# Performance work log

Measured on AMD Instinct MI355X. Metric: run time of the kernel, lower is better.

The kernel has to match this reference:

```python
import jax, jax.numpy as jnp
import numpy as np

B, P = 8, 768
S = 36                 # sample_points (also deformable offset pairs)
C_IN, C_ADJ = 64, 72   # prior_feat_channels -> adjusted channels
D, G = 512, 4          # fc_hidden_dim, num_groups (= attention heads)
N_OFFSETS, N_STRIPS, DEG = 72, 71, 3


def _bilinear(img, x, y):
    """img: [B,H,W,C]; x,y: [B,N] pixel coords. Bilinear sample, zeros outside."""
    H, W = img.shape[1], img.shape[2]
    x0 = jnp.floor(x); y0 = jnp.floor(y)
    x0i = x0.astype(jnp.int32); y0i = y0.astype(jnp.int32)
    wx1 = x - x0; wy1 = y - y0

    def corner(xi, yi, w):
        valid = (xi >= 0) & (xi < W) & (yi >= 0) & (yi < H)
        xc = jnp.clip(xi, 0, W - 1); yc = jnp.clip(yi, 0, H - 1)
        vals = jax.vmap(lambda f, yy, xx: f[yy, xx])(img, yc, xc)  # [B,N,C]
        return vals * (w * valid)[..., None]

    return (corner(x0i, y0i, (1 - wx1) * (1 - wy1))
            + corner(x0i + 1, y0i, wx1 * (1 - wy1))
            + corner(x0i, y0i + 1, (1 - wx1) * wy1)
            + corner(x0i + 1, y0i + 1, wx1 * wy1))


def _resize_ac(img, Ht, Wt):
    """Bilinear resize with align_corners=True. img: [B,H,W,C]."""
    Bsz, H, W, _ = img.shape
    gy, gx = jnp.meshgrid(jnp.linspace(0.0, H - 1.0, Ht),
                          jnp.linspace(0.0, W - 1.0, Wt), indexing='ij')
    xf = jnp.broadcast_to(gx.reshape(-1), (Bsz, Ht * Wt))
    yf = jnp.broadcast_to(gy.reshape(-1), (Bsz, Ht * Wt))
    return _bilinear(img, xf, yf).reshape(Bsz, Ht, Wt, -1)


def setup_inputs():
    ks = jax.random.split(jax.random.key(0), 32)
    r = lambda i, shp, s=1.0: jax.random.normal(ks[i], shp, dtype=jnp.float32) * s
    z = lambda shp: jnp.zeros(shp, jnp.float32)
    return {
        'feat0': r(0, (B, C_IN, 40, 100)),
        'feat1': r(1, (B, C_IN, 20, 50)),
        'feat2': r(2, (B, C_IN, 10, 25)),
        'priors': jax.random.uniform(ks[3], (B, P, 4 + N_OFFSETS), dtype=jnp.float32) * N_STRIPS,
        'ca_w': r(4, (C_ADJ, C_IN), 0.125), 'ca_b': z((C_ADJ,)),
        'off_w': r(5, (2 * S, C_ADJ), 0.01), 'off_b': r(6, (2 * S,), 0.01),
        'dp_w': r(7, (C_ADJ, C_ADJ), 0.167), 'dp_b': z((C_ADJ,)),
        'z_emb': r(8, (S,), 0.3) + 1.0,
        'gf_w': r(9, (D, S // G, C_ADJ), 0.02), 'gf_b': z((D,)),
        'wq': r(10, (D, D), 0.044), 'bq': z((D,)),
        'wk': r(11, (D, D), 0.044), 'bk': z((D,)),
        'wv': r(12, (D, D), 0.044), 'bv': z((D,)),
        'wo': r(13, (D, D), 0.044), 'bo': z((D,)),
        'cf_w1': r(14, (2 * D, D), 0.044), 'cf_b1': z((2 * D,)),
        'cf_w2': r(15, (D, 2 * D), 0.031), 'cf_b2': z((D,)),
        'cls_w1': r(16, (D, D), 0.044), 'cls_b1': z((D,)),
        'cls_w2': r(17, (2, D), 0.001), 'cls_b2': z((2,)),
        'reg_w1': r(18, (D, D), 0.044), 'reg_b1': z((D,)),
        'p_w1': r(19, (2 * D, D), 0.044), 'p_b1': z((2 * D,)),
        'p_w2': r(20, (DEG + 1, 2 * D), 0.031), 'p_b2': z((DEG + 1,)),
        'b_scale': jnp.ones((1,), jnp.float32), 'b_bias': z((1,)),
    }


def reference(feat0, feat1, feat2, priors, ca_w, ca_b, off_w, off_b, dp_w, dp_b,
              z_emb, gf_w, gf_b, wq, bq, wk, bk, wv, bv, wo, bo,
              cf_w1, cf_b1, cf_w2, cf_b2, cls_w1, cls_b1, cls_w2, cls_b2,
              reg_w1, reg_b1, p_w1, p_b1, p_w2, p_b2, b_scale, b_bias):
    f32 = jnp.float32
    lin = lambda x, w, b: x @ w.T + b

    # ---- prior sampling grid (CLRNet-style) ----
    sx_idx = jnp.floor(jnp.linspace(0.0, 1.0, S) * N_STRIPS).astype(jnp.int32)
    pf_ys = jnp.flip(1.0 - sx_idx.astype(f32) / N_STRIPS)            # [S]
    pf_xs = priors[..., 4 + sx_idx][:, :, ::-1]                       # [B,P,S]
    gx = jnp.clip(pf_xs / N_STRIPS, 0.0, 1.0) * 2.0 - 1.0            # [-1,1]
    gy = jnp.broadcast_to(pf_ys * 2.0 - 1.0, gx.shape)

    # ---- channel adjust (1x1 conv) per level, channels-last ----
    adj = lambda f: jnp.einsum('bchw,oc->bhwo', f, ca_w) + ca_b
    feats = [adj(feat0), adj(feat1), adj(feat2)]                      # [B,H,W,C_ADJ]
    offs0 = jnp.einsum('bhwc,oc->bhwo', feats[0], off_w) + off_b     # [B,H0,W0,2S]

    # ---- deformable multi-level sampling: per (prior, point) gather + 1x1 proj ----
    sidx = jnp.arange(S)
    levels = []
    for l, fl in enumerate(feats):
        Hl, Wl = fl.shape[1], fl.shape[2]
        offs = offs0 if l == 0 else _resize_ac(offs0, Hl, Wl)
        px = (gx + 1.0) * 0.5 * (Wl - 1)
        py = (gy + 1.0) * 0.5 * (Hl - 1)
        ov = _bilinear(offs, px.reshape(B, -1), py.reshape(B, -1)).reshape(B, P, S, S, 2)
        dyx = ov[:, :, sidx, sidx, :]                                 # offset pair s for point s
        sxp = (px + dyx[..., 1]).reshape(B, -1)
        syp = (py + dyx[..., 0]).reshape(B, -1)
        smp = _bilinear(fl, sxp, syp).reshape(B, P, S, C_ADJ)
        levels.append(smp @ dp_w.T + dp_b)
    feat_all = jnp.stack(levels)                                      # [3,B,P,S,C]

    # ---- z-embedding soft level selection ----
    zw = jax.nn.softmax(-(z_emb[:, None] - jnp.arange(3, dtype=f32)) ** 2 / 2.0, axis=-1)  # [S,3]
    feature = jnp.einsum('lbpsc,sl->bpsc', feat_all, zw)

    # ---- grouped gather Conv1d(S -> D, kernel=C_ADJ, groups=G) ----
    xg = feature.reshape(B * P, G, S // G, C_ADJ)
    wg = gf_w.reshape(G, D // G, S // G, C_ADJ)
    feature = (jnp.einsum('ngik,goik->ngo', xg, wg).reshape(B * P, D) + gf_b).reshape(B, P, D)

    # ---- multi-head self-attention over priors + channel MLP residual ----
    dh = D // G
    q = lin(feature, wq, bq).reshape(B, P, G, dh).transpose(0, 2, 1, 3)
    k = lin(feature, wk, bk).reshape(B, P, G, dh).transpose(0, 2, 1, 3)
    v = lin(feature, wv, bv).reshape(B, P, G, dh).transpose(0, 2, 1, 3)
    attn = jax.nn.softmax(jnp.einsum('bgqd,bgkd->bgqk', q, k) / float(np.sqrt(dh)), axis=-1)
    res = jnp.einsum('bgqk,bgkd->bgqd', attn, v).transpose(0, 2, 1, 3).reshape(B, P, D)
    res = lin(res, wo, bo)
    feature = feature + lin(jax.nn.relu(lin(res, cf_w1, cf_b1)), cf_w2, cf_b2)

    # ---- heads ----
    fc = feature.reshape(B * P, D)
    cls_logits = lin(jax.nn.relu(lin(fc, cls_w1, cls_b1)), cls_w2, cls_b2).reshape(B, P, 2)
    reg = jax.nn.relu(lin(fc, reg_w1, reg_b1)).reshape(B, P, D)
    coeffs = lin(jax.nn.relu(lin(reg, p_w1, p_b1)), p_w2, p_b2)       # [B,P,DEG+1]
    coeffs = jnp.concatenate([coeffs[..., :2], coeffs[..., 2:] * b_scale + b_bias], axis=-1)
    ys = jnp.linspace(0.0, 1.0, N_OFFSETS)
    basis = jnp.stack([ys ** i for i in range(DEG + 1)], axis=1)      # [N_OFFSETS, DEG+1]
    xs_pred = jax.nn.sigmoid(jnp.einsum('bnd,od->bno', coeffs, basis))
    return jnp.concatenate([cls_logits, coeffs, xs_pred], axis=-1)    # [B,P,78]
```

## Files before the change

### kernel.cpp

```cpp
#include <hip/hip_runtime.h>
#include <hip/hip_bf16.h>
#include <math.h>

#define BB 8
#define PP 768
#define NPRI 76
#define SS 36
#define CIN 64
#define CADJ 72
#define DD 512

#define H0 40
#define W0 100
#define H1 20
#define W1 50
#define H2 10
#define W2 25

typedef __attribute__((ext_vector_type(8))) short bf16x8;
typedef __attribute__((ext_vector_type(4))) short bf16x4;
typedef __attribute__((ext_vector_type(4))) float f32x4;
#define MFMA_BF16 __builtin_amdgcn_mfma_f32_16x16x32_bf16

typedef const __attribute__((address_space(1))) unsigned int* gas_t;
typedef __attribute__((address_space(3))) unsigned int* las_t;

__device__ __forceinline__ __hip_bfloat16 to_bf16(float v) { return __float2bfloat16(v); }
__device__ __forceinline__ float bf2f(__hip_bfloat16 v) { return __bfloat162float(v); }
__device__ __forceinline__ short to_bf16s(float v) {
    __hip_bfloat16 h = __float2bfloat16(v);
    return *reinterpret_cast<short*>(&h);
}
__device__ __forceinline__ float bfs2f(short s) {
    union { unsigned u; float f; } cv;
    cv.u = ((unsigned)(unsigned short)s) << 16;
    return cv.f;
}

__device__ __forceinline__ float bsample(const float* __restrict__ img, int H, int W,
                                         int C, int c, float x, float y)
{
    float x0f = floorf(x), y0f = floorf(y);
    int x0 = (int)x0f, y0 = (int)y0f;
    float wx1 = x - x0f, wy1 = y - y0f;
    float wx0 = 1.0f - wx1, wy0 = 1.0f - wy1;
    int xc0 = min(max(x0, 0), W - 1);
    int xc1 = min(max(x0 + 1, 0), W - 1);
    int yc0 = min(max(y0, 0), H - 1);
    int yc1 = min(max(y0 + 1, 0), H - 1);
    bool vx0 = (x0 >= 0) && (x0 < W);
    bool vx1 = (x0 + 1 >= 0) && (x0 + 1 < W);
    bool vy0 = (y0 >= 0) && (y0 < H);
    bool vy1 = (y0 + 1 >= 0) && (y0 + 1 < H);
    float w00 = (vx0 && vy0) ? wx0 * wy0 : 0.0f;
    float w01 = (vx1 && vy0) ? wx1 * wy0 : 0.0f;
    float w10 = (vx0 && vy1) ? wx0 * wy1 : 0.0f;
    float w11 = (vx1 && vy1) ? wx1 * wy1 : 0.0f;
    return w00 * img[((size_t)yc0 * W + xc0) * C + c]
         + w01 * img[((size_t)yc0 * W + xc1) * C + c]
         + w10 * img[((size_t)yc1 * W + xc0) * C + c]
         + w11 * img[((size_t)yc1 * W + xc1) * C + c];
}

__global__ __launch_bounds__(256) void k_wprep(
    const float* __restrict__ wq, const float* __restrict__ wk, const float* __restrict__ wv,
    const float* __restrict__ wo, const float* __restrict__ cf_w1, const float* __restrict__ cf_w2,
    const float* __restrict__ cls_w1, const float* __restrict__ reg_w1, const float* __restrict__ p_w1,
    const float* __restrict__ bq, const float* __restrict__ bk, const float* __restrict__ bv,
    const float* __restrict__ cls_b1, const float* __restrict__ reg_b1,
    const float* __restrict__ gf_w, const float* __restrict__ dp_w,
    const float* __restrict__ dp_b, const float* __restrict__ gf_b,
    __hip_bfloat16* __restrict__ wqkv, __hip_bfloat16* __restrict__ wo_bf,
    __hip_bfloat16* __restrict__ cf1_bf, __hip_bfloat16* __restrict__ cf2_bf,
    __hip_bfloat16* __restrict__ clsreg_bf, __hip_bfloat16* __restrict__ p1_bf,
    __hip_bfloat16* __restrict__ gfw2, float* __restrict__ b2,
    float* __restrict__ bqkv, float* __restrict__ bclsreg)
{
    __shared__ float dpS[CADJ][CADJ + 1];
    __shared__ float gfr[648];
    const int bid = blockIdx.x;
    const int tid = threadIdx.x;

    if (bid < 512) {
        const int o = bid;
        for (int i = tid; i < CADJ * CADJ; i += 256) dpS[i / CADJ][i % CADJ] = dp_w[i];
        for (int i = tid; i < 648; i += 256) gfr[i] = gf_w[(size_t)o * 648 + i];
        __syncthreads();
        for (int t = tid; t < 672; t += 256) {
            float acc = 0.0f;
            if (t < 648) {
                const int i = t / 72, m = t % 72;
                const float* gr = gfr + i * 72;
#pragma unroll 8
                for (int k = 0; k < 72; ++k) acc = fmaf(gr[k], dpS[k][m], acc);
            }
            gfw2[(size_t)o * 672 + t] = to_bf16(acc);
        }
        return;
    }
    if (bid < 514) {
        const int o = (bid - 512) * 256 + tid;
        if (o < DD) {
            const float* gr = gf_w + (size_t)o * 648;
            float acc = gf_b[o];
            for (int j = 0; j < 648; ++j) acc = fmaf(gr[j], dp_b[j % 72], acc);
            b2[o] = acc;
        }
        return;
    }
    long i = (long)(bid - 514) * 256 + tid;
    if (i < 262144) { wqkv[i] = to_bf16(wq[i]); return; }
    i -= 262144;
    if (i < 262144) { wqkv[262144 + i] = to_bf16(wk[i]); return; }
    i -= 262144;
    if (i < 262144) { wqkv[524288 + i] = to_bf16(wv[i]); return; }
    i -= 262144;
    if (i < 262144) { wo_bf[i] = to_bf16(wo[i]); return; }
    i -= 262144;
    if (i < 524288) { cf1_bf[i] = to_bf16(cf_w1[i]); return; }
    i -= 524288;
    if (i < 524288) { cf2_bf[i] = to_bf16(cf_w2[i]); return; }
    i -= 524288;
    if (i < 262144) { clsreg_bf[i] = to_bf16(cls_w1[i]); return; }
    i -= 262144;
    if (i < 262144) { clsreg_bf[262144 + i] = to_bf16(reg_w1[i]); return; }
    i -= 262144;
    if (i < 524288) { p1_bf[i] = to_bf16(p_w1[i]); return; }
    i -= 524288;
    if (i < 512) { bqkv[i] = bq[i]; return; }
    if (i < 1024) { bqkv[i] = bk[i - 512]; return; }
    if (i < 1536) { bqkv[i] = bv[i - 1024]; return; }
    i -= 1536;
    if (i < 512) { bclsreg[i] = cls_b1[i]; return; }
    if (i < 1024) { bclsreg[i] = reg_b1[i - 512]; return; }
}

__global__ __launch_bounds__(256) void k_adjoff(
    const float* __restrict__ f, const float* __restrict__ caw, const float* __restrict__ cab,
    const float* __restrict__ offw, const float* __restrict__ offb,
    __hip_bfloat16* __restrict__ feout, float* __restrict__ offout, int HW, int do_off)
{
    __shared__ float inS[64][65];
    __shared__ float wS[72][64];
    __shared__ float owS[72][73];
    __shared__ float feS[64][73];
    __shared__ float cabS[72], obS[72];

    const int tid = threadIdx.x;
    const int b = blockIdx.y;
    const int pix0 = blockIdx.x * 64;
    const int cnt = min(64, HW - pix0);
    const int px = tid & 63, og = tid >> 6, o0 = og * 18;

    const float* fb = f + (size_t)b * CIN * HW + pix0;
    for (int i = tid; i < 72 * 64; i += 256) wS[i >> 6][i & 63] = caw[i];
    if (do_off)
        for (int i = tid; i < 72 * 72; i += 256) owS[i / 72][i % 72] = offw[i];
    if (tid < 72) { cabS[tid] = cab[tid]; obS[tid] = do_off ? offb[tid] : 0.f; }
    for (int i = tid; i < 64 * 64; i += 256) {
        const int c = i >> 6, p = i & 63;
        inS[c][p] = (p < cnt) ? fb[(size_t)c * HW + p] : 0.f;
    }
    __syncthreads();

    float acc[18];
#pragma unroll
    for (int j = 0; j < 18; ++j) acc[j] = cabS[o0 + j];
#pragma unroll 4
    for (int c = 0; c < 64; ++c) {
        const float v = inS[c][px];
#pragma unroll
        for (int j = 0; j < 18; ++j) acc[j] = fmaf(v, wS[o0 + j][c], acc[j]);
    }
#pragma unroll
    for (int j = 0; j < 18; ++j) feS[px][o0 + j] = acc[j];
    __syncthreads();

    __hip_bfloat16* feg = feout + ((size_t)b * HW + pix0) * CADJ;
    for (int i = tid; i < cnt * CADJ; i += 256) feg[i] = to_bf16(feS[i / CADJ][i % CADJ]);

    if (!do_off) return;

    float acc2[18];
#pragma unroll
    for (int j = 0; j < 18; ++j) acc2[j] = obS[o0 + j];
#pragma unroll 4
    for (int c = 0; c < 72; ++c) {
        const float v = feS[px][c];
#pragma unroll
        for (int j = 0; j < 18; ++j) acc2[j] = fmaf(v, owS[o0 + j][c], acc2[j]);
    }
    __syncthreads();
#pragma unroll
    for (int j = 0; j < 18; ++j) feS[px][o0 + j] = acc2[j];
    __syncthreads();
    float* ofg = offout + ((size_t)b * HW + pix0) * CADJ;
    for (int i = tid; i < cnt * CADJ; i += 256) ofg[i] = feS[i / CADJ][i % CADJ];
}

__global__ __launch_bounds__(256) void k_resize2(const float* __restrict__ src,
    float* __restrict__ of1, float* __restrict__ of2)
{
    const int T1 = BB * H1 * W1 * CADJ;
    const int T2 = BB * H2 * W2 * CADJ;
    int idx = blockIdx.x * 256 + threadIdx.x;
    if (idx < T1) {
        const int c = idx % CADJ;
        const int j = (idx / CADJ) % W1;
        const int i = (idx / (CADJ * W1)) % H1;
        const int b = idx / (CADJ * W1 * H1);
        float sy = fminf((float)i * ((float)(H0 - 1) / (float)(H1 - 1)), (float)(H0 - 1));
        float sx = fminf((float)j * ((float)(W0 - 1) / (float)(W1 - 1)), (float)(W0 - 1));
        of1[idx] = bsample(src + (size_t)b * H0 * W0 * CADJ, H0, W0, CADJ, c, sx, sy);
        return;
    }
    idx -= T1;
    if (idx >= T2) return;
    const int c = idx % CADJ;
    const int j = (idx / CADJ) % W2;
    const int i = (idx / (CADJ * W2)) % H2;
    const int b = idx / (CADJ * W2 * H2);
    float sy = fminf((float)i * ((float)(H0 - 1) / (float)(H2 - 1)), (float)(H0 - 1));
    float sx = fminf((float)j * ((float)(W0 - 1) / (float)(W2 - 1)), (float)(W0 - 1));
    of2[idx] = bsample(src + (size_t)b * H0 * W0 * CADJ, H0, W0, CADJ, c, sx, sy);
}

__global__ __launch_bounds__(256) void k_sample(
    const float* __restrict__ priors,
    const __hip_bfloat16* __restrict__ feats0, const __hip_bfloat16* __restrict__ feats1,
    const __hip_bfloat16* __restrict__ feats2,
    const float* __restrict__ offs0,  const float* __restrict__ offs1,  const float* __restrict__ offs2,
    const float* __restrict__ z_emb,
    __hip_bfloat16* __restrict__ fsout)
{
    const int bid = blockIdx.x;
    const int gi = (bid & 7) * 384 + (bid >> 3);
    const int bp0 = gi * 2;
    const int b = bp0 / PP;
    const int tid = threadIdx.x;

    __shared__ int   ib[2][3][SS][4];
    __shared__ float wz[2][3][SS][4];

    const int Hs[3] = {H0, H1, H2};
    const int Wsz[3] = {W0, W1, W2};
    const __hip_bfloat16* Fb[3] = { feats0 + (size_t)b * H0 * W0 * CADJ,
                                    feats1 + (size_t)b * H1 * W1 * CADJ,
                                    feats2 + (size_t)b * H2 * W2 * CADJ };
    const float* Ob[3] = { offs0 + (size_t)b * H0 * W0 * CADJ,
                           offs1 + (size_t)b * H1 * W1 * CADJ,
                           offs2 + (size_t)b * H2 * W2 * CADJ };

    if (tid < 2 * 3 * SS) {
        const int p = tid / 108;
        const int l = (tid % 108) / SS;
        const int s = tid % SS;
        const int bp = bp0 + p;
        const float t = (float)(35 - s) / 35.0f;
        const int m = (int)floorf(t * 71.0f);
        const float pfx = priors[(size_t)bp * NPRI + 4 + m];
        const float gxv = fminf(fmaxf(pfx / 71.0f, 0.0f), 1.0f) * 2.0f - 1.0f;
        const float gyv = (1.0f - (float)m / 71.0f) * 2.0f - 1.0f;
        const float z = z_emb[s];
        const float e0 = expf(-0.5f * z * z);
        const float e1 = expf(-0.5f * (z - 1.0f) * (z - 1.0f));
        const float e2 = expf(-0.5f * (z - 2.0f) * (z - 2.0f));
        const float inv = 1.0f / (e0 + e1 + e2);
        const float ev[3] = {e0, e1, e2};
        const float zwl = ev[l] * inv;

        const int Hl = Hs[l], Wl = Wsz[l];
        const float px = (gxv + 1.0f) * 0.5f * (float)(Wl - 1);
        const float py = (gyv + 1.0f) * 0.5f * (float)(Hl - 1);
        const float dy = bsample(Ob[l], Hl, Wl, CADJ, 2 * s,     px, py);
        const float dx = bsample(Ob[l], Hl, Wl, CADJ, 2 * s + 1, px, py);
        const float sx = px + dx, sy = py + dy;
        const float x0f = floorf(sx), y0f = floorf(sy);
        const int x0 = (int)x0f, y0 = (int)y0f;
        const float wx1 = sx - x0f, wy1 = sy - y0f;
        const float wx0 = 1.0f - wx1, wy0 = 1.0f - wy1;
        const bool vx0 = (x0 >= 0) && (x0 < Wl);
        const bool vx1 = (x0 + 1 >= 0) && (x0 + 1 < Wl);
        const bool vy0 = (y0 >= 0) && (y0 < Hl);
        const bool vy1 = (y0 + 1 >= 0) && (y0 + 1 < Hl);
        const int xc0 = min(max(x0, 0), Wl - 1);
        const int xc1 = min(max(x0 + 1, 0), Wl - 1);
        const int yc0 = min(max(y0, 0), Hl - 1);
        const int yc1 = min(max(y0 + 1, 0), Hl - 1);
        wz[p][l][s][0] = ((vx0 && vy0) ? wx0 * wy0 : 0.0f) * zwl;
        wz[p][l][s][1] = ((vx1 && vy0) ? wx1 * wy0 : 0.0f) * zwl;
        wz[p][l][s][2] = ((vx0 && vy1) ? wx0 * wy1 : 0.0f) * zwl;
        wz[p][l][s][3] = ((vx1 && vy1) ? wx1 * wy1 : 0.0f) * zwl;
        ib[p][l][s][0] = (yc0 * Wl + xc0) * CADJ;
        ib[p][l][s][1] = (yc0 * Wl + xc1) * CADJ;
        ib[p][l][s][2] = (yc1 * Wl + xc0) * CADJ;
        ib[p][l][s][3] = (yc1 * Wl + xc1) * CADJ;
    }
    __syncthreads();

    for (int idx = tid; idx < 2 * SS * 18; idx += 256) {
        const int p = idx / 648;
        const int rem = idx % 648;
        const int s = rem / 18, k4 = (rem % 18) * 4;
        float a0 = 0.f, a1 = 0.f, a2 = 0.f, a3 = 0.f;
#pragma unroll
        for (int l = 0; l < 3; ++l) {
            const __hip_bfloat16* F = Fb[l];
            const int*   ibs = ib[p][l][s];
            const float* ws  = wz[p][l][s];
#pragma unroll
            for (int c = 0; c < 4; ++c) {
                const bf16x4 v = *(const bf16x4*)(F + ibs[c] + k4);
                const float w = ws[c];
                a0 = fmaf(w, bfs2f(v[0]), a0);
                a1 = fmaf(w, bfs2f(v[1]), a1);
                a2 = fmaf(w, bfs2f(v[2]), a2);
                a3 = fmaf(w, bfs2f(v[3]), a3);
            }
        }
        bf16x4 pk;
        pk[0] = to_bf16s(a0); pk[1] = to_bf16s(a1);
        pk[2] = to_bf16s(a2); pk[3] = to_bf16s(a3);
        __hip_bfloat16* orow = fsout + (size_t)(bp0 + p) * 2688;
        *(bf16x4*)&orow[(s / 9) * 672 + (s % 9) * 72 + k4] = pk;
    }
    if (tid < 2 * 96) {
        const int p = tid / 96, g = (tid % 96) / 24, t = tid % 24;
        fsout[(size_t)(bp0 + p) * 2688 + g * 672 + 648 + t] = to_bf16(0.0f);
    }
}

__global__ __launch_bounds__(256) void k_bgemm(
    const __hip_bfloat16* __restrict__ A, int lda, long sAz,
    const __hip_bfloat16* __restrict__ W, int ldw, long sWz,
    const float* __restrict__ bias, int sBz,
    const __hip_bfloat16* __restrict__ Res, int ldres,
    __hip_bfloat16* __restrict__ C, int ldc, int sCz,
    int K, int relu)
{
    __shared__ __hip_bfloat16 As[128][32];
    __shared__ __hip_bfloat16 Bs[128][32];
    const int tid = threadIdx.x;
    const int lane = tid & 63, w = tid >> 6;
    const int wr = w >> 1, wc = w & 1;
    const int row16 = lane & 15, kg = lane >> 4;
    const int z = blockIdx.z;
    const int m0 = blockIdx.y * 128, n0 = blockIdx.x * 128;
    const __hip_bfloat16* Ab = A + (size_t)z * sAz;
    const __hip_bfloat16* Wb = W + (size_t)z * sWz;
    const int gr = lane >> 2;
    const int gc = (lane & 3) * 8;

    f32x4 acc[4][4];
#pragma unroll
    for (int i = 0; i < 4; ++i)
#pragma unroll
        for (int j = 0; j < 4; ++j) acc[i][j] = (f32x4){0.f, 0.f, 0.f, 0.f};

    for (int k0 = 0; k0 < K; k0 += 32) {
        __syncthreads();
#pragma unroll
        for (int c = 0; c < 2; ++c) {
            const int r = w * 32 + c * 16;
            __builtin_amdgcn_global_load_lds(
                (gas_t)(Ab + (size_t)(m0 + r + gr) * lda + k0 + gc),
                (las_t)&As[r][0], 16, 0, 0);
            __builtin_amdgcn_global_load_lds(
                (gas_t)(Wb + (size_t)(n0 + r + gr) * ldw + k0 + gc),
                (las_t)&Bs[r][0], 16, 0, 0);
        }
        __syncthreads();
        bf16x8 af[4], bfr[4];
#pragma unroll
        for (int i = 0; i < 4; ++i) af[i]  = *(const bf16x8*)&As[wr * 64 + i * 16 + row16][kg * 8];
#pragma unroll
        for (int j = 0; j < 4; ++j) bfr[j] = *(const bf16x8*)&Bs[wc * 64 + j * 16 + row16][kg * 8];
#pragma unroll
        for (int i = 0; i < 4; ++i)
#pragma unroll
            for (int j = 0; j < 4; ++j)
                acc[i][j] = MFMA_BF16(af[i], bfr[j], acc[i][j], 0, 0, 0);
    }

    const float* bz = bias + (size_t)z * sBz;
    __hip_bfloat16* Cz = C + (size_t)z * sCz;
#pragma unroll
    for (int i = 0; i < 4; ++i) {
#pragma unroll
        for (int r = 0; r < 4; ++r) {
            const int row = m0 + wr * 64 + i * 16 + kg * 4 + r;
#pragma unroll
            for (int j = 0; j < 4; ++j) {
                const int col = n0 + wc * 64 + j * 16 + row16;
                float v = acc[i][j][r] + bz[col];
                if (Res) v += bf2f(Res[(size_t)row * ldres + col]);
                if (relu) v = fmaxf(v, 0.0f);
                Cz[(size_t)row * ldc + col] = to_bf16(v);
            }
        }
    }
}

__global__ __launch_bounds__(256) void k_bgemm64(
    const __hip_bfloat16* __restrict__ A, int lda, long sAz,
    const __hip_bfloat16* __restrict__ W, int ldw, long sWz,
    const float* __restrict__ bias, int sBz,
    const __hip_bfloat16* __restrict__ Res, int ldres,
    __hip_bfloat16* __restrict__ C, int ldc, int sCz,
    int K, int relu)
{
    __shared__ __hip_bfloat16 As[2][64][32];
    __shared__ __hip_bfloat16 Bs[2][64][32];
    const int tid = threadIdx.x;
    const int lane = tid & 63, w = tid >> 6;
    const int wr = w >> 1, wc = w & 1;
    const int row16 = lane & 15, kg = lane >> 4;
    const int z = blockIdx.z;
    const int m0 = blockIdx.y * 64, n0 = blockIdx.x * 64;
    const __hip_bfloat16* Ab = A + (size_t)z * sAz;
    const __hip_bfloat16* Wb = W + (size_t)z * sWz;
    const int gr = lane >> 2;
    const int gc = (lane & 3) * 8;

    f32x4 acc[2][2];
#pragma unroll
    for (int i = 0; i < 2; ++i)
#pragma unroll
        for (int j = 0; j < 2; ++j) acc[i][j] = (f32x4){0.f, 0.f, 0.f, 0.f};

    __builtin_amdgcn_global_load_lds(
        (gas_t)(Ab + (size_t)(m0 + w * 16 + gr) * lda + gc),
        (las_t)&As[0][w * 16][0], 16, 0, 0);
    __builtin_amdgcn_global_load_lds(
        (gas_t)(Wb + (size_t)(n0 + w * 16 + gr) * ldw + gc),
        (las_t)&Bs[0][w * 16][0], 16, 0, 0);
    __syncthreads();

    int cur = 0;
    for (int k0 = 0; k0 < K; k0 += 32) {
        if (k0 + 32 < K) {
            const int nxt = cur ^ 1;
            __builtin_amdgcn_global_load_lds(
                (gas_t)(Ab + (size_t)(m0 + w * 16 + gr) * lda + k0 + 32 + gc),
                (las_t)&As[nxt][w * 16][0], 16, 0, 0);
            __builtin_amdgcn_global_load_lds(
                (gas_t)(Wb + (size_t)(n0 + w * 16 + gr) * ldw + k0 + 32 + gc),
                (las_t)&Bs[nxt][w * 16][0], 16, 0, 0);
        }
        bf16x8 af[2], bfr[2];
#pragma unroll
        for (int i = 0; i < 2; ++i) af[i]  = *(const bf16x8*)&As[cur][wr * 32 + i * 16 + row16][kg * 8];
#pragma unroll
        for (int j = 0; j < 2; ++j) bfr[j] = *(const bf16x8*)&Bs[cur][wc * 32 + j * 16 + row16][kg * 8];
#pragma unroll
        for (int i = 0; i < 2; ++i)
#pragma unroll
            for (int j = 0; j < 2; ++j)
                acc[i][j] = MFMA_BF16(af[i], bfr[j], acc[i][j], 0, 0, 0);
        __syncthreads();
        cur ^= 1;
    }

    const float* bz = bias + (size_t)z * sBz;
    __hip_bfloat16* Cz = C + (size_t)z * sCz;
#pragma unroll
    for (int i = 0; i < 2; ++i) {
#pragma unroll
        for (int r = 0; r < 4; ++r) {
            const int row = m0 + wr * 32 + i * 16 + kg * 4 + r;
#pragma unroll
            for (int j = 0; j < 2; ++j) {
                const int col = n0 + wc * 32 + j * 16 + row16;
                float v = acc[i][j][r] + bz[col];
                if (Res) v += bf2f(Res[(size_t)row * ldres + col]);
                if (relu) v = fmaxf(v, 0.0f);
                Cz[(size_t)row * ldc + col] = to_bf16(v);
            }
        }
    }
}

__global__ __launch_bounds__(256) void k_vt(
    const __hip_bfloat16* __restrict__ qkv, __hip_bfloat16* __restrict__ Vt)
{
    const int kt = blockIdx.x;
    const int bg = blockIdx.y;
    const int b = bg >> 2, g = bg & 3;
    const int tid = threadIdx.x;
    __shared__ unsigned short Vs[64][130];

    const __hip_bfloat16* src = qkv + (size_t)(b * PP + kt * 64) * 1536 + 1024 + g * 128;
    for (int i = tid; i < 1024; i += 256) {
        const int row = i >> 4, ch = i & 15;
        *(bf16x8*)&Vs[row][ch * 8] = *(const bf16x8*)(src + (size_t)row * 1536 + ch * 8);
    }
    __syncthreads();
    __hip_bfloat16* dst = Vt + (size_t)bg * 128 * 768 + kt * 64;
    for (int i = tid; i < 1024; i += 256) {
        const int d = i >> 3, kc = i & 7;
        bf16x8 pk;
#pragma unroll
        for (int j = 0; j < 8; ++j) pk[j] = (short)Vs[kc * 8 + j][d];
        *(bf16x8*)(dst + (size_t)d * 768 + kc * 8) = pk;
    }
}

__global__ __launch_bounds__(256) void k_fattn(
    const __hip_bfloat16* __restrict__ qkv, const __hip_bfloat16* __restrict__ Vt,
    __hip_bfloat16* __restrict__ Out)
{
    const int id = blockIdx.x;
    const int xcd = id & 7, rest = id >> 3;
    const int bg = xcd * 4 + rest / 12;
    const int qt = rest % 12;
    const int b = bg >> 2, g = bg & 3;
    const int tid = threadIdx.x, lane = tid & 63, w = tid >> 6;
    const int row16 = lane & 15, kg = lane >> 4;
    const int q0 = qt * 64;

    __shared__ __hip_bfloat16 Klds[64][136];
    __shared__ __hip_bfloat16 Vtl[128][72];
    __shared__ __hip_bfloat16 Plds[4][16][72];

    const size_t rowQ = (size_t)(b * PP + q0 + w * 16 + row16) * 1536 + g * 128;
    bf16x8 aq[4];
#pragma unroll
    for (int t = 0; t < 4; ++t)
        aq[t] = *(const bf16x8*)(qkv + rowQ + t * 32 + kg * 8);

    f32x4 oacc[8];
#pragma unroll
    for (int dt = 0; dt < 8; ++dt) oacc[dt] = (f32x4){0.f, 0.f, 0.f, 0.f};
    float mrow[4] = {-3.0e38f, -3.0e38f, -3.0e38f, -3.0e38f};
    float lrow[4] = {0.f, 0.f, 0.f, 0.f};

    const __hip_bfloat16* Kb = qkv + (size_t)(b * PP) * 1536 + 512 + g * 128;
    const __hip_bfloat16* Vb = Vt + (size_t)bg * 128 * 768;
    const float sc = 0.08838834764831845f;

    const int krow = tid >> 2, kch = tid & 3;
    const int vrow = tid >> 1, vch = tid & 1;
    bf16x8 kreg[4], vreg[4];

    {
        const __hip_bfloat16* s1 = Kb + (size_t)krow * 1536 + kch * 32;
        const __hip_bfloat16* s2 = Vb + (size_t)vrow * 768 + vch * 32;
#pragma unroll
        for (int j = 0; j < 4; ++j) { kreg[j] = *(const bf16x8*)(s1 + j * 8);
                                      vreg[j] = *(const bf16x8*)(s2 + j * 8); }
    }

    for (int kt = 0; kt < 12; ++kt) {
        __syncthreads();
#pragma unroll
        for (int j = 0; j < 4; ++j) {
            *(bf16x8*)&Klds[krow][kch * 32 + j * 8] = kreg[j];
            *(bf16x8*)&Vtl[vrow][vch * 32 + j * 8] = vreg[j];
        }
        __syncthreads();
        if (kt < 11) {
            const __hip_bfloat16* s1 = Kb + (size_t)((kt + 1) * 64 + krow) * 1536 + kch * 32;
            const __hip_bfloat16* s2 = Vb + (size_t)vrow * 768 + (kt + 1) * 64 + vch * 32;
#pragma unroll
            for (int j = 0; j < 4; ++j) { kreg[j] = *(const bf16x8*)(s1 + j * 8);
                                          vreg[j] = *(const bf16x8*)(s2 + j * 8); }
        }

        f32x4 s4[4];
#pragma unroll
        for (int st = 0; st < 4; ++st) s4[st] = (f32x4){0.f, 0.f, 0.f, 0.f};
        __builtin_amdgcn_s_setprio(1);
#pragma unroll
        for (int st = 0; st < 4; ++st)
#pragma unroll
            for (int t = 0; t < 4; ++t)
                s4[st] = MFMA_BF16(aq[t],
                    *(const bf16x8*)&Klds[st * 16 + row16][t * 32 + kg * 8], s4[st], 0, 0, 0);
        __builtin_amdgcn_s_setprio(0);

        float pm[4];
#pragma unroll
        for (int r = 0; r < 4; ++r) {
            float m0 = fmaxf(fmaxf(s4[0][r], s4[1][r]), fmaxf(s4[2][r], s4[3][r])) * sc;
            m0 = fmaxf(m0, __shfl_xor(m0, 1));
            m0 = fmaxf(m0, __shfl_xor(m0, 2));
            m0 = fmaxf(m0, __shfl_xor(m0, 4));
            m0 = fmaxf(m0, __shfl_xor(m0, 8));
            pm[r] = m0;
        }
        const float need = fmaxf(fmaxf(pm[0] - mrow[0], pm[1] - mrow[1]),
                                 fmaxf(pm[2] - mrow[2], pm[3] - mrow[3]));
        if (!__all(need <= 8.0f)) {
#pragma unroll
            for (int r = 0; r < 4; ++r) {
                const float mn = fmaxf(mrow[r], pm[r]);
                const float so = __expf(mrow[r] - mn);
                lrow[r] *= so;
#pragma unroll
                for (int dt = 0; dt < 8; ++dt) oacc[dt][r] *= so;
                mrow[r] = mn;
            }
        }
#pragma unroll
        for (int r = 0; r < 4; ++r) {
            float rs = 0.f;
#pragma unroll
            for (int st = 0; st < 4; ++st) {
                const float p = __expf(s4[st][r] * sc - mrow[r]);
                rs += p;
                Plds[w][kg * 4 + r][st * 16 + row16] = to_bf16(p);
            }
            rs += __shfl_xor(rs, 1);
            rs += __shfl_xor(rs, 2);
            rs += __shfl_xor(rs, 4);
            rs += __shfl_xor(rs, 8);
            lrow[r] += rs;
        }

        __builtin_amdgcn_s_setprio(1);
#pragma unroll
        for (int ks = 0; ks < 2; ++ks) {
            bf16x8 ap = *(const bf16x8*)&Plds[w][row16][ks * 32 + kg * 8];
#pragma unroll
            for (int dt = 0; dt < 8; ++dt)
                oacc[dt] = MFMA_BF16(ap,
                    *(const bf16x8*)&Vtl[dt * 16 + row16][ks * 32 + kg * 8], oacc[dt], 0, 0, 0);
        }
        __builtin_amdgcn_s_setprio(0);
    }

    const size_t obase = (size_t)(b * PP + q0 + w * 16 + kg * 4) * DD + g * 128;
#pragma unroll
    for (int r = 0; r < 4; ++r) {
        const float inv = 1.0f / lrow[r];
#pragma unroll
        for (int dt = 0; dt < 8; ++dt)
            Out[obase + (size_t)r * DD + dt * 16 + row16] = to_bf16(oacc[dt][r] * inv);
    }
}

__global__ __launch_bounds__(64) void k_head(
    const __hip_bfloat16* __restrict__ clsreg, const __hip_bfloat16* __restrict__ ph,
    const float* __restrict__ cls_w2, const float* __restrict__ cls_b2,
    const float* __restrict__ p_w2, const float* __restrict__ p_b2,
    const float* __restrict__ b_scale, const float* __restrict__ b_bias,
    float* __restrict__ outp)
{
    const int bp = blockIdx.x;
    const int lane = threadIdx.x;
    const __hip_bfloat16* hr = clsreg + (size_t)bp * 1024;
    float a0 = 0.0f, a1 = 0.0f;
    for (int i = lane; i < DD; i += 64) {
        float h = bf2f(hr[i]);
        a0 = fmaf(h, cls_w2[i], a0);
        a1 = fmaf(h, cls_w2[DD + i], a1);
    }
    const __hip_bfloat16* pr = ph + (size_t)bp * 1024;
    float c0 = 0.0f, c1 = 0.0f, c2 = 0.0f, c3 = 0.0f;
    for (int i = lane; i < 1024; i += 64) {
        float h = bf2f(pr[i]);
        c0 = fmaf(h, p_w2[i], c0);
        c1 = fmaf(h, p_w2[1024 + i], c1);
        c2 = fmaf(h, p_w2[2048 + i], c2);
        c3 = fmaf(h, p_w2[3072 + i], c3);
    }
#pragma unroll
    for (int off = 32; off > 0; off >>= 1) {
        a0 += __shfl_down(a0, off);
        a1 += __shfl_down(a1, off);
        c0 += __shfl_down(c0, off);
        c1 += __shfl_down(c1, off);
        c2 += __shfl_down(c2, off);
        c3 += __shfl_down(c3, off);
    }
    a0 = __shfl(a0, 0); a1 = __shfl(a1, 0);
    c0 = __shfl(c0, 0); c1 = __shfl(c1, 0);
    c2 = __shfl(c2, 0); c3 = __shfl(c3, 0);
    const float k0 = c0 + p_b2[0];
    const float k1 = c1 + p_b2[1];
    const float scv = b_scale[0], biv = b_bias[0];
    const float k2 = (c2 + p_b2[2]) * scv + biv;
    const float k3 = (c3 + p_b2[3]) * scv + biv;
    float* orow = outp + (size_t)bp * 78;
    if (lane == 0) {
        orow[0] = a0 + cls_b2[0];
        orow[1] = a1 + cls_b2[1];
        orow[2] = k0; orow[3] = k1; orow[4] = k2; orow[5] = k3;
    }
    for (int o = lane; o < 72; o += 64) {
        float ys = (float)o / 71.0f;
        float tv = k0 + ys * (k1 + ys * (k2 + ys * k3));
        orow[6 + o] = 1.0f / (1.0f + expf(-tv));
    }
}

extern "C" void kernel_launch(void* const* d_in, const int* in_sizes, int n_in,
                              void* d_out, int out_size, void* d_ws, size_t ws_size,
                              hipStream_t stream)
{
    const float* feat0  = (const float*)d_in[0];
    const float* feat1  = (const float*)d_in[1];
    const float* feat2  = (const float*)d_in[2];
    const float* priors = (const float*)d_in[3];
    const float* ca_w   = (const float*)d_in[4];
    const float* ca_b   = (const float*)d_in[5];
    const float* off_w  = (const float*)d_in[6];
    const float* off_b  = (const float*)d_in[7];
    const float* dp_w   = (const float*)d_in[8];
    const float* dp_b   = (const float*)d_in[9];
    const float* z_emb  = (const float*)d_in[10];
    const float* gf_w   = (const float*)d_in[11];
    const float* gf_b   = (const float*)d_in[12];
    const float* wq     = (const float*)d_in[13];
    const float* bq     = (const float*)d_in[14];
    const float* wk     = (const float*)d_in[15];
    const float* bk     = (const float*)d_in[16];
    const float* wv     = (const float*)d_in[17];
    const float* bv     = (const float*)d_in[18];
    const float* wo     = (const float*)d_in[19];
    const float* bo     = (const float*)d_in[20];
    const float* cf_w1  = (const float*)d_in[21];
    const float* cf_b1  = (const float*)d_in[22];
    const float* cf_w2  = (const float*)d_in[23];
    const float* cf_b2  = (const float*)d_in[24];
    const float* cls_w1 = (const float*)d_in[25];
    const float* cls_b1 = (const float*)d_in[26];
    const float* cls_w2 = (const float*)d_in[27];
    const float* cls_b2 = (const float*)d_in[28];
    const float* reg_w1 = (const float*)d_in[29];
    const float* reg_b1 = (const float*)d_in[30];
    const float* p_w1   = (const float*)d_in[31];
    const float* p_b1   = (const float*)d_in[32];
    const float* p_w2   = (const float*)d_in[33];
    const float* p_b2   = (const float*)d_in[34];
    const float* b_scale = (const float*)d_in[35];
    const float* b_bias  = (const float*)d_in[36];
    float* out = (float*)d_out;

    char* wsb = (char*)d_ws;
    __hip_bfloat16* feature = (__hip_bfloat16*)(wsb + 0);
    __hip_bfloat16* qkvb    = (__hip_bfloat16*)(wsb + 6291456);
    __hip_bfloat16* tb      = (__hip_bfloat16*)(wsb + 25165824);
    __hip_bfloat16* vtb     = (__hip_bfloat16*)(wsb + 31457280);
    __hip_bfloat16* rb      = (__hip_bfloat16*)(wsb + 31457280);
    __hip_bfloat16* hb      = (__hip_bfloat16*)(wsb + 37748736);
    __hip_bfloat16* f2      = (__hip_bfloat16*)(wsb + 50331648);
    __hip_bfloat16* clsregb = (__hip_bfloat16*)(wsb + 56623104);
    __hip_bfloat16* phb     = (__hip_bfloat16*)(wsb + 69206016);
    float* of1 = (float*)(wsb + 6291456);
    float* of2 = (float*)(wsb + 8595456);
    __hip_bfloat16* fe1 = (__hip_bfloat16*)(wsb + 9171456);
    __hip_bfloat16* fe2 = (__hip_bfloat16*)(wsb + 11475456);
    __hip_bfloat16* fsb = (__hip_bfloat16*)(wsb + 25165824);
    __hip_bfloat16* fe0 = (__hip_bfloat16*)(wsb + 58195968);
    float* of0 = (float*)(wsb + 67411968);
    __hip_bfloat16* wqkv_bf   = (__hip_bfloat16*)(wsb + 81788928);
    __hip_bfloat16* wo_bf     = (__hip_bfloat16*)(wsb + 83361792);
    __hip_bfloat16* cf1_bf    = (__hip_bfloat16*)(wsb + 83886080);
    __hip_bfloat16* cf2_bf    = (__hip_bfloat16*)(wsb + 84934656);
    __hip_bfloat16* clsreg_bf = (__hip_bfloat16*)(wsb + 85983232);
    __hip_bfloat16* p1_bf     = (__hip_bfloat16*)(wsb + 87031808);
    __hip_bfloat16* gfw2_bf   = (__hip_bfloat16*)(wsb + 88080384);
    float* bqkv    = (float*)(wsb + 88768512);
    float* bclsreg = (float*)(wsb + 88774656);
    float* b2      = (float*)(wsb + 88778752);

    k_wprep<<<12812, 256, 0, stream>>>(
        wq, wk, wv, wo, cf_w1, cf_w2, cls_w1, reg_w1, p_w1, bq, bk, bv, cls_b1, reg_b1,
        gf_w, dp_w, dp_b, gf_b,
        wqkv_bf, wo_bf, cf1_bf, cf2_bf, clsreg_bf, p1_bf, gfw2_bf, b2, bqkv, bclsreg);

    k_adjoff<<<dim3(63, BB), 256, 0, stream>>>(feat0, ca_w, ca_b, off_w, off_b,
                                               fe0, of0, H0 * W0, 1);
    k_adjoff<<<dim3(16, BB), 256, 0, stream>>>(feat1, ca_w, ca_b, off_w, off_b,
                                               fe1, nullptr, H1 * W1, 0);
    k_adjoff<<<dim3(4, BB), 256, 0, stream>>>(feat2, ca_w, ca_b, off_w, off_b,
                                              fe2, nullptr, H2 * W2, 0);
    k_resize2<<<(BB * (H1 * W1 + H2 * W2) * CADJ + 255) / 256, 256, 0, stream>>>(of0, of1, of2);
    k_sample<<<3072, 256, 0, stream>>>(priors, fe0, fe1, fe2, of0, of1, of2, z_emb, fsb);

    const int M = BB * PP;
    k_bgemm64<<<dim3(2, M / 64, 4), 256, 0, stream>>>(
        fsb, 2688, 672, gfw2_bf, 672, 128 * 672, b2, 128,
        nullptr, 0, feature, DD, 128, 672, 0);
    k_bgemm<<<dim3(12, M / 128, 1), 256, 0, stream>>>(
        feature, DD, 0, wqkv_bf, DD, 0, bqkv, 0,
        nullptr, 0, qkvb, 1536, 0, DD, 0);
    k_vt<<<dim3(12, 32), 256, 0, stream>>>(qkvb, vtb);
    k_fattn<<<384, 256, 0, stream>>>(qkvb, vtb, tb);
    k_bgemm64<<<dim3(8, M / 64, 1), 256, 0, stream>>>(
        tb, DD, 0, wo_bf, DD, 0, bo, 0, nullptr, 0, rb, DD, 0, DD, 0);
    k_bgemm64<<<dim3(16, M / 64, 1), 256, 0, stream>>>(
        rb, DD, 0, cf1_bf, DD, 0, cf_b1, 0, nullptr, 0, hb, 1024, 0, DD, 1);
    k_bgemm64<<<dim3(8, M / 64, 1), 256, 0, stream>>>(
        hb, 1024, 0, cf2_bf, 1024, 0, cf_b2, 0, feature, DD, f2, DD, 0, 1024, 0);
    k_bgemm64<<<dim3(16, M / 64, 1), 256, 0, stream>>>(
        f2, DD, 0, clsreg_bf, DD, 0, bclsreg, 0, nullptr, 0, clsregb, 1024, 0, DD, 1);
    k_bgemm64<<<dim3(16, M / 64, 1), 256, 0, stream>>>(
        clsregb + 512, 1024, 0, p1_bf, DD, 0, p_b1, 0, nullptr, 0, phb, 1024, 0, DD, 1);

    k_head<<<M, 64, 0, stream>>>(clsregb, phb, cls_w2, cls_b2, p_w2, p_b2, b_scale, b_bias, out);
}
```

Measured before the change: 299.3 us.

## Double-buffer bgemm LDS staging, fuse level-1/2 channel adjust, vectorize sample loads

The 128x128 MFMA GEMM now double-buffers its LDS tiles, issuing the next k-slab's global-to-LDS loads before computing on the current one and dropping one barrier per iteration. Levels 1 and 2 of the channel-adjust projection are merged into a new k_adj12 kernel, which saves a launch and skips the unused offset branch. The sampling kernel reads the four corner indices and weights as aligned int4/float4 vectors from shared memory. Costs are twice the LDS per GEMM block, which may reduce occupancy, and whether a single barrier per iteration correctly orders the async LDS writes.

```diff
diff --git a/kernel.cpp b/kernel.cpp
--- a/kernel.cpp
+++ b/kernel.cpp
@@ -198,6 +198,53 @@
     for (int i = tid; i < cnt * CADJ; i += 256) ofg[i] = feS[i / CADJ][i % CADJ];
 }
 
+__global__ __launch_bounds__(256) void k_adj12(
+    const float* __restrict__ f1, const float* __restrict__ f2,
+    const float* __restrict__ caw, const float* __restrict__ cab,
+    __hip_bfloat16* __restrict__ fe1, __hip_bfloat16* __restrict__ fe2)
+{
+    __shared__ float inS[64][65];
+    __shared__ float wS[72][64];
+    __shared__ float feS[64][73];
+    __shared__ float cabS[72];
+
+    const int tid = threadIdx.x;
+    const int b = blockIdx.y;
+    const int bx = blockIdx.x;
+    const float* f;
+    __hip_bfloat16* fe;
+    int HW, pix0;
+    if (bx < 16) { f = f1; fe = fe1; HW = H1 * W1; pix0 = bx * 64; }
+    else         { f = f2; fe = fe2; HW = H2 * W2; pix0 = (bx - 16) * 64; }
+    const int cnt = min(64, HW - pix0);
+    const int px = tid & 63, og = tid >> 6, o0 = og * 18;
+
+    const float* fb = f + (size_t)b * CIN * HW + pix0;
+    for (int i = tid; i < 72 * 64; i += 256) wS[i >> 6][i & 63] = caw[i];
+    if (tid < 72) cabS[tid] = cab[tid];
+    for (int i = tid; i < 64 * 64; i += 256) {
+        const int c = i >> 6, p = i & 63;
+        inS[c][p] = (p < cnt) ? fb[(size_t)c * HW + p] : 0.f;
+    }
+    __syncthreads();
+
+    float acc[18];
+#pragma unroll
+    for (int j = 0; j < 18; ++j) acc[j] = cabS[o0 + j];
+#pragma unroll 4
+    for (int c = 0; c < 64; ++c) {
+        const float v = inS[c][px];
+#pragma unroll
+        for (int j = 0; j < 18; ++j) acc[j] = fmaf(v, wS[o0 + j][c], acc[j]);
+    }
+#pragma unroll
+    for (int j = 0; j < 18; ++j) feS[px][o0 + j] = acc[j];
+    __syncthreads();
+
+    __hip_bfloat16* feg = fe + ((size_t)b * HW + pix0) * CADJ;
+    for (int i = tid; i < cnt * CADJ; i += 256) feg[i] = to_bf16(feS[i / CADJ][i % CADJ]);
+}
+
 __global__ __launch_bounds__(256) void k_resize2(const float* __restrict__ src,
     float* __restrict__ of1, float* __restrict__ of2)
 {
@@ -239,8 +286,8 @@
     const int b = bp0 / PP;
     const int tid = threadIdx.x;
 
-    __shared__ int   ib[2][3][SS][4];
-    __shared__ float wz[2][3][SS][4];
+    __shared__ __align__(16) int   ib[2][3][SS][4];
+    __shared__ __align__(16) float wz[2][3][SS][4];
 
     const int Hs[3] = {H0, H1, H2};
     const int Wsz[3] = {W0, W1, W2};
@@ -306,17 +353,20 @@
 #pragma unroll
         for (int l = 0; l < 3; ++l) {
             const __hip_bfloat16* F = Fb[l];
-            const int*   ibs = ib[p][l][s];
-            const float* ws  = wz[p][l][s];
-#pragma unroll
-            for (int c = 0; c < 4; ++c) {
-                const bf16x4 v = *(const bf16x4*)(F + ibs[c] + k4);
-                const float w = ws[c];
-                a0 = fmaf(w, bfs2f(v[0]), a0);
-                a1 = fmaf(w, bfs2f(v[1]), a1);
-                a2 = fmaf(w, bfs2f(v[2]), a2);
-                a3 = fmaf(w, bfs2f(v[3]), a3);
-            }
+            const int4   i4 = *(const int4*)&ib[p][l][s][0];
+            const float4 w4 = *(const float4*)&wz[p][l][s][0];
+            const bf16x4 v0 = *(const bf16x4*)(F + i4.x + k4);
+            const bf16x4 v1 = *(const bf16x4*)(F + i4.y + k4);
+            const bf16x4 v2 = *(const bf16x4*)(F + i4.z + k4);
+            const bf16x4 v3 = *(const bf16x4*)(F + i4.w + k4);
+            a0 = fmaf(w4.x, bfs2f(v0[0]), a0); a1 = fmaf(w4.x, bfs2f(v0[1]), a1);
+            a2 = fmaf(w4.x, bfs2f(v0[2]), a2); a3 = fmaf(w4.x, bfs2f(v0[3]), a3);
+            a0 = fmaf(w4.y, bfs2f(v1[0]), a0); a1 = fmaf(w4.y, bfs2f(v1[1]), a1);
+            a2 = fmaf(w4.y, bfs2f(v1[2]), a2); a3 = fmaf(w4.y, bfs2f(v1[3]), a3);
+            a0 = fmaf(w4.z, bfs2f(v2[0]), a0); a1 = fmaf(w4.z, bfs2f(v2[1]), a1);
+            a2 = fmaf(w4.z, bfs2f(v2[2]), a2); a3 = fmaf(w4.z, bfs2f(v2[3]), a3);
+            a0 = fmaf(w4.w, bfs2f(v3[0]), a0); a1 = fmaf(w4.w, bfs2f(v3[1]), a1);
+            a2 = fmaf(w4.w, bfs2f(v3[2]), a2); a3 = fmaf(w4.w, bfs2f(v3[3]), a3);
         }
         bf16x4 pk;
         pk[0] = to_bf16s(a0); pk[1] = to_bf16s(a1);
@@ -338,8 +388,8 @@
     __hip_bfloat16* __restrict__ C, int ldc, int sCz,
     int K, int relu)
 {
-    __shared__ __hip_bfloat16 As[128][32];
-    __shared__ __hip_bfloat16 Bs[128][32];
+    __shared__ __hip_bfloat16 As[2][128][32];
+    __shared__ __hip_bfloat16 Bs[2][128][32];
     const int tid = threadIdx.x;
     const int lane = tid & 63, w = tid >> 6;
     const int wr = w >> 1, wc = w & 1;
@@ -351,36 +401,46 @@
     const int gr = lane >> 2;
     const int gc = (lane & 3) * 8;
 
+#define STAGE128(buf, kbase)                                                       \
+    {                                                                              \
+        _Pragma("unroll")                                                          \
+        for (int c = 0; c < 2; ++c) {                                              \
+            const int r = w * 32 + c * 16;                                         \
+            __builtin_amdgcn_global_load_lds(                                      \
+                (gas_t)(Ab + (size_t)(m0 + r + gr) * lda + (kbase) + gc),          \
+                (las_t)&As[buf][r][0], 16, 0, 0);                                  \
+            __builtin_amdgcn_global_load_lds(                                      \
+                (gas_t)(Wb + (size_t)(n0 + r + gr) * ldw + (kbase) + gc),          \
+                (las_t)&Bs[buf][r][0], 16, 0, 0);                                  \
+        }                                                                          \
+    }
+
     f32x4 acc[4][4];
 #pragma unroll
     for (int i = 0; i < 4; ++i)
 #pragma unroll
         for (int j = 0; j < 4; ++j) acc[i][j] = (f32x4){0.f, 0.f, 0.f, 0.f};
 
+    STAGE128(0, 0)
+    __syncthreads();
+
+    int cur = 0;
     for (int k0 = 0; k0 < K; k0 += 32) {
-        __syncthreads();
-#pragma unroll
-        for (int c = 0; c < 2; ++c) {
-            const int r = w * 32 + c * 16;
-            __builtin_amdgcn_global_load_lds(
-                (gas_t)(Ab + (size_t)(m0 + r + gr) * lda + k0 + gc),
-                (las_t)&As[r][0], 16, 0, 0);
-            __builtin_amdgcn_global_load_lds(
-                (gas_t)(Wb + (size_t)(n0 + r + gr) * ldw + k0 + gc),
-                (las_t)&Bs[r][0], 16, 0, 0);
-        }
-        __syncthreads();
+        if (k0 + 32 < K) STAGE128(cur ^ 1, k0 + 32)
         bf16x8 af[4], bfr[4];
 #pragma unroll
-        for (int i = 0; i < 4; ++i) af[i]  = *(const bf16x8*)&As[wr * 64 + i * 16 + row16][kg * 8];
-#pragma unroll
-        for (int j = 0; j < 4; ++j) bfr[j] = *(const bf16x8*)&Bs[wc * 64 + j * 16 + row16][kg * 8];
+        for (int i = 0; i < 4; ++i) af[i]  = *(const bf16x8*)&As[cur][wr * 64 + i * 16 + row16][kg * 8];
+#pragma unroll
+        for (int j = 0; j < 4; ++j) bfr[j] = *(const bf16x8*)&Bs[cur][wc * 64 + j * 16 + row16][kg * 8];
 #pragma unroll
         for (int i = 0; i < 4; ++i)
 #pragma unroll
             for (int j = 0; j < 4; ++j)
                 acc[i][j] = MFMA_BF16(af[i], bfr[j], acc[i][j], 0, 0, 0);
-    }
+        __syncthreads();
+        cur ^= 1;
+    }
+#undef STAGE128
 
     const float* bz = bias + (size_t)z * sBz;
     __hip_bfloat16* Cz = C + (size_t)z * sCz;
@@ -772,10 +832,7 @@
 
     k_adjoff<<<dim3(63, BB), 256, 0, stream>>>(feat0, ca_w, ca_b, off_w, off_b,
                                                fe0, of0, H0 * W0, 1);
-    k_adjoff<<<dim3(16, BB), 256, 0, stream>>>(feat1, ca_w, ca_b, off_w, off_b,
-                                               fe1, nullptr, H1 * W1, 0);
-    k_adjoff<<<dim3(4, BB), 256, 0, stream>>>(feat2, ca_w, ca_b, off_w, off_b,
-                                              fe2, nullptr, H2 * W2, 0);
+    k_adj12<<<dim3(20, BB), 256, 0, stream>>>(feat1, feat2, ca_w, ca_b, fe1, fe2);
     k_resize2<<<(BB * (H1 * W1 + H2 * W2) * CADJ + 255) / 256, 256, 0, stream>>>(of0, of1, of2);
     k_sample<<<3072, 256, 0, stream>>>(priors, fe0, fe1, fe2, of0, of1, of2, z_emb, fsb);
 
```

New measurement: 284.9 us. -4.8%, faster.
